# Kernel tuning notes

Hardware: AMD Instinct MI355X
Metric: run time of the kernel (lower is better)

Reference implementation:

```python
import jax, jax.numpy as jnp
import numpy as np

B, M, D, H = 2, 2048, 1024, 16


def _rope(x):
    # Equivalent to x.transpose(0,1) @ R[:m] with R the block-diagonal 2x2
    # rotation matrices from get_rotary_matrix (note the (i-1) in theta,
    # faithful to the source).
    b, m, d = x.shape
    i = jnp.arange(d // 2, dtype=jnp.float32)
    theta = 10000.0 ** (-2.0 * (i - 1.0) / d)           # [d/2]
    ang = jnp.arange(m, dtype=jnp.float32)[:, None] * theta[None, :]  # [m, d/2]
    c, s = jnp.cos(ang), jnp.sin(ang)
    xe, xo = x[..., 0::2], x[..., 1::2]                 # [b, m, d/2]
    ye = xe * c + xo * s                                # out[2i]   = q[2i]*cos + q[2i+1]*sin
    yo = -xe * s + xo * c                               # out[2i+1] = -q[2i]*sin + q[2i+1]*cos
    return jnp.stack([ye, yo], axis=-1).reshape(b, m, d)


def setup_inputs() -> dict:
    key = jax.random.key(0)
    ks = jax.random.split(key, 8)
    w = lambda k, shape: (jax.random.normal(k, shape, jnp.float32) * 0.02)
    return {
        "x": jax.random.normal(ks[0], (B, M, D), jnp.float32),
        "wq": w(ks[1], (D, D)),
        "wk": w(ks[2], (D, D)),
        "wv": w(ks[3], (D, D)),
        "in_proj_w": w(ks[4], (3 * D, D)),
        "in_proj_b": w(ks[5], (3 * D,)),
        "out_w": w(ks[6], (D, D)),
        "out_b": w(ks[7], (D,)),
    }


def reference(x, wq, wk, wv, in_proj_w, in_proj_b, out_w, out_b):
    b, m, d = x.shape
    h = H
    hd = d // h
    # bias-free QKV projections, each followed by the dense RoPE rotation
    q = _rope(x @ wq.T)
    k = _rope(x @ wk.T)
    v = _rope(x @ wv.T)
    # nn.MultiheadAttention: packed in_proj, scaled dot-product, causal mask, out_proj
    wqi, wki, wvi = jnp.split(in_proj_w, 3, axis=0)
    bqi, bki, bvi = jnp.split(in_proj_b, 3, axis=0)
    qh = (q @ wqi.T + bqi).reshape(b, m, h, hd)
    kh = (k @ wki.T + bki).reshape(b, m, h, hd)
    vh = (v @ wvi.T + bvi).reshape(b, m, h, hd)
    scores = jnp.einsum("bqhd,bkhd->bhqk", qh, kh) / jnp.sqrt(jnp.float32(hd))
    causal = jnp.tril(jnp.ones((m, m), dtype=bool))
    scores = jnp.where(causal, scores, jnp.float32(-jnp.inf))
    attn = jax.nn.softmax(scores, axis=-1)              # dropout p=0.0
    o = jnp.einsum("bhqk,bkhd->bqhd", attn, vh).reshape(b, m, d)
    return o @ out_w.T + out_b
```

## Files before the change

kernel.cpp:

```cpp
#include <hip/hip_runtime.h>
#include <hip/hip_bf16.h>
#include <math.h>

typedef __bf16 bf16;
typedef __bf16 bf16x4 __attribute__((ext_vector_type(4)));
typedef __bf16 bf16x8 __attribute__((ext_vector_type(8)));
typedef float  f32x4  __attribute__((ext_vector_type(4)));

#define MM 2048
#define DD 1024
#define HD 64

__device__ __forceinline__ void gload16(const void* g, void* l) {
  __builtin_amdgcn_global_load_lds((const __attribute__((address_space(1))) void*)g,
                                   (__attribute__((address_space(3))) void*)l, 16, 0, 0);
}

__global__ __launch_bounds__(256) void k_cvt_all(
    const float* __restrict__ x,   const float* __restrict__ wq,
    const float* __restrict__ wk,  const float* __restrict__ wv,
    const float* __restrict__ ipw, const float* __restrict__ ow,
    bf16* __restrict__ xb,  bf16* __restrict__ wqb, bf16* __restrict__ wkb,
    bf16* __restrict__ wvb, bf16* __restrict__ ipwb, bf16* __restrict__ owb)
{
  int bid = blockIdx.x;
  const float* s; bf16* d; int base;
  if (bid < 4096)       { s = x;   d = xb;   base = bid; }
  else if (bid < 5120)  { s = wq;  d = wqb;  base = bid - 4096; }
  else if (bid < 6144)  { s = wk;  d = wkb;  base = bid - 5120; }
  else if (bid < 7168)  { s = wv;  d = wvb;  base = bid - 6144; }
  else if (bid < 10240) { s = ipw; d = ipwb; base = bid - 7168; }
  else                  { s = ow;  d = owb;  base = bid - 10240; }
  int i = base*256 + threadIdx.x;
  float4 v = ((const float4*)s)[i];
  bf16x4 o;
  o[0]=(bf16)v.x; o[1]=(bf16)v.y; o[2]=(bf16)v.z; o[3]=(bf16)v.w;
  ((bf16x4*)d)[i] = o;
}

__device__ __forceinline__ void gemm_core8(const bf16* __restrict__ A,
                                           const bf16* __restrict__ Bw,
                                           const int row0, const int col0,
                                           bf16* __restrict__ sA, bf16* __restrict__ sB,
                                           f32x4 (&acc)[2][4])
{
  const int t = threadIdx.x;
  #pragma unroll
  for (int m=0;m<2;m++)
    #pragma unroll
    for (int n=0;n<4;n++)
      acc[m][n] = (f32x4){0.f,0.f,0.f,0.f};

  const int srow = t >> 3;
  const int lch  = ((t & 7) - (srow & 7)) & 7;
  const bf16* gA = A  + (size_t)(row0 + srow)*DD + lch*8;
  const bf16* gB = Bw + (size_t)(col0 + srow)*DD + lch*8;
  char* lA = (char*)sA + t*16;
  char* lB = (char*)sB + t*16;

  const int lane = t & 63, wid = t >> 6;
  const int wr = wid >> 1, wc = wid & 1;
  const int fr = lane & 15, fg = lane >> 4;
  const int fr7 = fr & 7;

  gload16(gA,                 lA);
  gload16(gA + (size_t)64*DD, lA + 8192);
  gload16(gB,                 lB);
  gload16(gB + (size_t)64*DD, lB + 8192);

  for (int kt = 0; kt < 16; ++kt) {
    const int buf = kt & 1;
    __builtin_amdgcn_s_barrier();
    if (kt < 15) {
      const int nb = buf ^ 1;
      const int ko = (kt + 1) * 64;
      gload16(gA + ko,                 lA + nb*16384);
      gload16(gA + (size_t)64*DD + ko, lA + nb*16384 + 8192);
      gload16(gB + ko,                 lB + nb*16384);
      gload16(gB + (size_t)64*DD + ko, lB + nb*16384 + 8192);
      asm volatile("s_waitcnt vmcnt(4)" ::: "memory");
    } else {
      asm volatile("s_waitcnt vmcnt(0)" ::: "memory");
    }
    __builtin_amdgcn_s_barrier();
    const char* bA = (const char*)sA + buf*16384;
    const char* bB = (const char*)sB + buf*16384;
    bf16x8 aF[2][2], bF[2][4];
    #pragma unroll
    for (int kb=0;kb<2;kb++) {
      #pragma unroll
      for (int m=0;m<2;m++)
        aF[kb][m] = *(const bf16x8*)(bA + (wr*32 + m*16 + fr)*128 + ((kb*4 + fg + fr7)&7)*16);
      #pragma unroll
      for (int n=0;n<4;n++)
        bF[kb][n] = *(const bf16x8*)(bB + (wc*64 + n*16 + fr)*128 + ((kb*4 + fg + fr7)&7)*16);
    }
    __builtin_amdgcn_s_setprio(1);
    #pragma unroll
    for (int kb=0;kb<2;kb++)
      #pragma unroll
      for (int m=0;m<2;m++)
        #pragma unroll
        for (int n=0;n<4;n++)
          acc[m][n] = __builtin_amdgcn_mfma_f32_16x16x32_bf16(aF[kb][m], bF[kb][n], acc[m][n], 0, 0, 0);
    __builtin_amdgcn_s_setprio(0);
  }
}

__global__ __launch_bounds__(512, 2) void k_gemm_rope(
    const bf16* __restrict__ X, const bf16* __restrict__ Wq,
    const bf16* __restrict__ Wk, const bf16* __restrict__ Wv,
    bf16* __restrict__ QKV)
{
  __shared__ bf16 sA[2*128*64];
  __shared__ bf16 sB[2*128*64];
  const int row0 = blockIdx.x * 128;
  const int col0 = blockIdx.y * 128;
  const int z = blockIdx.z;
  const bf16* Bw = (z==0) ? Wq : ((z==1) ? Wk : Wv);
  f32x4 acc[2][4];
  gemm_core8(X, Bw, row0, col0, sA, sB, acc);

  bf16* outp = QKV + (size_t)z * (4096u*1024u);
  const int lane = threadIdx.x & 63, wid = threadIdx.x >> 6;
  const int wr = wid >> 1, wc = wid & 1;
  const int fr = lane & 15, fg = lane >> 4;
  #pragma unroll
  for (int n=0;n<4;n++) {
    const int gc = col0 + wc*64 + n*16 + fr;
    const int i2 = gc >> 1;
    const float theta = __expf(((float)i2 - 1.0f) * (-2.0f * 9.210340371976184f / 1024.0f));
    #pragma unroll
    for (int m=0;m<2;m++) {
      #pragma unroll
      for (int r=0;r<4;r++) {
        const int gr = row0 + wr*32 + m*16 + fg*4 + r;
        const float v  = acc[m][n][r];
        const float pv = __shfl_xor(v, 1);
        const int pos = gr & (MM-1);
        float sv, cv;
        __sincosf((float)pos * theta, &sv, &cv);
        const float res = (gc & 1) ? (v*cv - pv*sv) : (v*cv + pv*sv);
        outp[(size_t)gr * DD + gc] = (bf16)res;
      }
    }
  }
}

__global__ __launch_bounds__(512, 2) void k_gemm_proj(
    const bf16* __restrict__ QKV, const bf16* __restrict__ IPW,
    const float* __restrict__ IPB,
    bf16* __restrict__ QH, bf16* __restrict__ KH, bf16* __restrict__ VT)
{
  __shared__ bf16 sA[2*128*64];
  __shared__ bf16 sB[2*128*64];
  const int row0 = blockIdx.x * 128;
  const int col0 = blockIdx.y * 128;
  const int z = blockIdx.z;
  const bf16* A  = QKV + (size_t)z * (4096u*1024u);
  const bf16* Bw = IPW + (size_t)z * (1024u*1024u);
  const float* bias = IPB + z * DD;
  f32x4 acc[2][4];
  gemm_core8(A, Bw, row0, col0, sA, sB, acc);

  const int lane = threadIdx.x & 63, wid = threadIdx.x >> 6;
  const int wr = wid >> 1, wc = wid & 1;
  const int fr = lane & 15, fg = lane >> 4;
  if (z < 2) {
    bf16* outp = (z==0) ? QH : KH;
    const float vscale = (z==0) ? 0.18033688011112042f : 1.0f;
    #pragma unroll
    for (int n=0;n<4;n++) {
      const int gc = col0 + wc*64 + n*16 + fr;
      const float bs = bias[gc];
      #pragma unroll
      for (int m=0;m<2;m++) {
        #pragma unroll
        for (int r=0;r<4;r++) {
          const int gr = row0 + wr*32 + m*16 + fg*4 + r;
          outp[(size_t)gr * DD + gc] = (bf16)((acc[m][n][r] + bs) * vscale);
        }
      }
    }
  } else {
    #pragma unroll
    for (int n=0;n<4;n++) {
      const int gc = col0 + wc*64 + n*16 + fr;
      const float bs = bias[gc];
      #pragma unroll
      for (int m=0;m<2;m++) {
        const int gr0 = row0 + wr*32 + m*16 + fg*4;
        const int b  = gr0 >> 11;
        const int m0 = gr0 & (MM-1);
        bf16x4 pk;
        #pragma unroll
        for (int r=0;r<4;r++) pk[r] = (bf16)(acc[m][n][r] + bs);
        *(bf16x4*)(VT + ((size_t)b*DD + gc)*MM + m0) = pk;
      }
    }
  }
}

__global__ __launch_bounds__(256) void k_attn(
    const bf16* __restrict__ QH, const bf16* __restrict__ KH,
    const bf16* __restrict__ VT, bf16* __restrict__ O)
{
  __shared__ bf16 sK[2*64*64];
  __shared__ bf16 sV[2*64*64];
  __shared__ bf16 sP[4*16*64];
  const int idx = blockIdx.x;
  const int xcd = idx & 7;
  const int rr  = idx >> 3;
  const int combo = xcd*4 + (rr & 3);
  const int b = combo >> 4, h = combo & 15;
  const int qt = 31 - (rr >> 2);
  const int t = threadIdx.x, lane = t & 63, wid = t >> 6;
  const int fr = lane & 15, fg = lane >> 4;
  const int swzP = (fr & 7) << 4;
  const int q0 = qt * 64;
  const int qg = q0 + wid*16 + fr;

  const int srow = t >> 3;
  const int cc   = (t & 7) ^ (srow & 7);
  const bf16* gK0 = KH + ((size_t)b*MM + srow)*DD + h*HD + cc*8;
  const bf16* gK1 = gK0 + (size_t)32*DD;
  const bf16* gV0 = VT + ((size_t)b*DD + h*HD + srow)*MM + cc*8;
  const bf16* gV1 = gV0 + (size_t)32*MM;
  char* lK = (char*)sK + t*16;
  char* lV = (char*)sV + t*16;
  char* sPw = (char*)(sP + wid*16*64);

  const bf16* qp = QH + ((size_t)b*MM + qg)*DD + h*HD + fg*8;
  bf16x8 aQ0 = *(const bf16x8*)qp;
  bf16x8 aQ1 = *(const bf16x8*)(qp + 32);

  bf16x8 ones;
  #pragma unroll
  for (int j=0;j<8;j++) ones[j] = (bf16)1.0f;

  gload16(gK0, lK);  gload16(gK1, lK + 4096);
  gload16(gV0, lV);  gload16(gV1, lV + 4096);

  f32x4 o_acc[4];
  #pragma unroll
  for (int n=0;n<4;n++) o_acc[n] = (f32x4){0.f,0.f,0.f,0.f};
  f32x4 lacc = (f32x4){0.f,0.f,0.f,0.f};
  const f32x4 minit = (f32x4){-32.f,-32.f,-32.f,-32.f};

  for (int kt = 0; kt <= qt; ++kt) {
    const int buf = kt & 1;
    asm volatile("s_waitcnt vmcnt(0)" ::: "memory");
    __builtin_amdgcn_s_barrier();
    if (kt < qt) {
      const int nb = buf ^ 1;
      gload16(gK0 + (size_t)(kt+1)*64*DD, lK + nb*8192);
      gload16(gK1 + (size_t)(kt+1)*64*DD, lK + nb*8192 + 4096);
      gload16(gV0 + (kt+1)*64,            lV + nb*8192);
      gload16(gV1 + (kt+1)*64,            lV + nb*8192 + 4096);
    }
    const char* bKb = (const char*)sK + buf*8192;
    const char* bVb = (const char*)sV + buf*8192;

    f32x4 sacc[4];
    #pragma unroll
    for (int n=0;n<4;n++) sacc[n] = minit;
    __builtin_amdgcn_s_setprio(1);
    #pragma unroll
    for (int kb=0;kb<2;kb++) {
      const bf16x8 q = kb ? aQ1 : aQ0;
      #pragma unroll
      for (int n=0;n<4;n++) {
        const int rowA = n*16 + fr;
        bf16x8 aK = *(const bf16x8*)(bKb + rowA*128 + ((kb*64 + fg*16) ^ ((rowA&7)<<4)));
        sacc[n] = __builtin_amdgcn_mfma_f32_16x16x32_bf16(aK, q, sacc[n], 0, 0, 0);
      }
    }
    __builtin_amdgcn_s_setprio(0);

    const bool diag = (kt == qt);
    float ps[16];
    #pragma unroll
    for (int n=0;n<4;n++)
      #pragma unroll
      for (int r=0;r<4;r++) {
        float xx = sacc[n][r];
        if (diag) {
          const int kvg = kt*64 + n*16 + fg*4 + r;
          if (kvg > qg) xx = -INFINITY;
        }
        ps[n*4+r] = exp2f(xx);
      }
    #pragma unroll
    for (int n=0;n<4;n++) {
      bf16x4 pk;
      #pragma unroll
      for (int r=0;r<4;r++) pk[r] = (bf16)ps[n*4+r];
      *(bf16x4*)(sPw + fr*128 + ((n*32 + fg*8) ^ swzP)) = pk;
    }
    asm volatile("s_waitcnt lgkmcnt(0)" ::: "memory");

    bf16x8 aP0 = *(const bf16x8*)(sPw + fr*128 + ((fg*16) ^ swzP));
    bf16x8 aP1 = *(const bf16x8*)(sPw + fr*128 + ((64 + fg*16) ^ swzP));
    __builtin_amdgcn_s_setprio(1);
    #pragma unroll
    for (int n=0;n<4;n++) {
      const int rowV = n*16 + fr;
      bf16x8 bV0 = *(const bf16x8*)(bVb + rowV*128 + ((fg*16) ^ ((rowV&7)<<4)));
      bf16x8 bV1 = *(const bf16x8*)(bVb + rowV*128 + ((64 + fg*16) ^ ((rowV&7)<<4)));
      o_acc[n] = __builtin_amdgcn_mfma_f32_16x16x32_bf16(aP0, bV0, o_acc[n], 0, 0, 0);
      o_acc[n] = __builtin_amdgcn_mfma_f32_16x16x32_bf16(aP1, bV1, o_acc[n], 0, 0, 0);
    }
    lacc = __builtin_amdgcn_mfma_f32_16x16x32_bf16(aP0, ones, lacc, 0, 0, 0);
    lacc = __builtin_amdgcn_mfma_f32_16x16x32_bf16(aP1, ones, lacc, 0, 0, 0);
    __builtin_amdgcn_s_setprio(0);
  }

  #pragma unroll
  for (int r=0;r<4;r++) {
    const int qq = q0 + wid*16 + fg*4 + r;
    const float inv = 1.0f / lacc[r];
    #pragma unroll
    for (int n=0;n<4;n++) {
      O[((size_t)b*MM + qq)*DD + h*HD + n*16 + fr] = (bf16)(o_acc[n][r] * inv);
    }
  }
}

__global__ __launch_bounds__(512, 2) void k_gemm_out(
    const bf16* __restrict__ A, const bf16* __restrict__ OW,
    const float* __restrict__ OBIAS, float* __restrict__ outp)
{
  __shared__ bf16 sA[2*128*64];
  __shared__ bf16 sB[2*128*64];
  const int row0 = blockIdx.x * 128;
  const int col0 = blockIdx.y * 128;
  f32x4 acc[2][4];
  gemm_core8(A, OW, row0, col0, sA, sB, acc);
  const int lane = threadIdx.x & 63, wid = threadIdx.x >> 6;
  const int wr = wid >> 1, wc = wid & 1;
  const int fr = lane & 15, fg = lane >> 4;
  #pragma unroll
  for (int n=0;n<4;n++) {
    const int gc = col0 + wc*64 + n*16 + fr;
    const float bs = OBIAS[gc];
    #pragma unroll
    for (int m=0;m<2;m++) {
      #pragma unroll
      for (int r=0;r<4;r++) {
        const int gr = row0 + wr*32 + m*16 + fg*4 + r;
        outp[(size_t)gr * DD + gc] = acc[m][n][r] + bs;
      }
    }
  }
}

extern "C" void kernel_launch(void* const* d_in, const int* in_sizes, int n_in,
                              void* d_out, int out_size, void* d_ws, size_t ws_size,
                              hipStream_t stream)
{
  (void)in_sizes; (void)n_in; (void)out_size; (void)ws_size;
  const float* x   = (const float*)d_in[0];
  const float* wq  = (const float*)d_in[1];
  const float* wk  = (const float*)d_in[2];
  const float* wv  = (const float*)d_in[3];
  const float* ipw = (const float*)d_in[4];
  const float* ipb = (const float*)d_in[5];
  const float* ow  = (const float*)d_in[6];
  const float* ob  = (const float*)d_in[7];
  float* outp = (float*)d_out;

  char* ws = (char*)d_ws;
  const size_t MB = 1u << 20;
  bf16* xb   = (bf16*)(ws + 0*MB);
  bf16* wqb  = (bf16*)(ws + 8*MB);
  bf16* wkb  = (bf16*)(ws + 10*MB);
  bf16* wvb  = (bf16*)(ws + 12*MB);
  bf16* ipwb = (bf16*)(ws + 14*MB);
  bf16* owb  = (bf16*)(ws + 20*MB);
  bf16* QKV  = (bf16*)(ws + 22*MB);
  bf16* QH   = (bf16*)(ws + 46*MB);
  bf16* KH   = (bf16*)(ws + 54*MB);
  bf16* VT   = (bf16*)(ws + 62*MB);
  bf16* Ob   = (bf16*)(ws + 70*MB);

  k_cvt_all<<<11264, 256, 0, stream>>>(x, wq, wk, wv, ipw, ow,
                                       xb, wqb, wkb, wvb, ipwb, owb);
  k_gemm_rope<<<dim3(32,8,3), 512, 0, stream>>>(xb, wqb, wkb, wvb, QKV);
  k_gemm_proj<<<dim3(32,8,3), 512, 0, stream>>>(QKV, ipwb, ipb, QH, KH, VT);
  k_attn<<<1024, 256, 0, stream>>>(QH, KH, VT, Ob);
  k_gemm_out<<<dim3(32,8,1), 512, 0, stream>>>(Ob, owb, ob, outp);
}
```

Measured before the change: 128.7 us.

## Split long causal attention query tiles into two KV halves with merge kernel

Query tiles 16-31 now have their KV loop split at tile 16 into two blocks, each writing unnormalised fp32 partial outputs and row sums to a workspace that reuses the QKV buffer. A new merge kernel sums the two partials and normalises them. The aim is to balance the causal workload across more blocks (1536 instead of 1024) and shorten the critical path of the longest tiles. The cost is an extra kernel launch and fp32 partial traffic. The merge is valid because the softmax uses a fixed max offset rather than a running max.

```diff
diff --git a/kernel.cpp b/kernel.cpp
--- a/kernel.cpp
+++ b/kernel.cpp
@@ -203,7 +203,8 @@
 
 __global__ __launch_bounds__(256) void k_attn(
     const bf16* __restrict__ QH, const bf16* __restrict__ KH,
-    const bf16* __restrict__ VT, bf16* __restrict__ O)
+    const bf16* __restrict__ VT, bf16* __restrict__ O,
+    float* __restrict__ pOut)
 {
   __shared__ bf16 sK[2*64*64];
   __shared__ bf16 sV[2*64*64];
@@ -213,7 +214,13 @@
   const int rr  = idx >> 3;
   const int combo = xcd*4 + (rr & 3);
   const int b = combo >> 4, h = combo & 15;
-  const int qt = 31 - (rr >> 2);
+  const int u = rr >> 2;
+  int qt, kt0, ktEnd, mode, slot = 0;
+  if (u < 16)      { qt = 16 + u; kt0 = 0;  ktEnd = 15; mode = 1;
+                     slot = (combo*16 + u)*2; }
+  else if (u < 32) { qt = 31 - u; kt0 = 0;  ktEnd = qt; mode = 0; }
+  else             { qt = 63 - u; kt0 = 16; ktEnd = qt; mode = 1;
+                     slot = (combo*16 + (qt-16))*2 + 1; }
   const int t = threadIdx.x, lane = t & 63, wid = t >> 6;
   const int fr = lane & 15, fg = lane >> 4;
   const int swzP = (fr & 7) << 4;
@@ -238,8 +245,8 @@
   #pragma unroll
   for (int j=0;j<8;j++) ones[j] = (bf16)1.0f;
 
-  gload16(gK0, lK);  gload16(gK1, lK + 4096);
-  gload16(gV0, lV);  gload16(gV1, lV + 4096);
+  gload16(gK0 + (size_t)kt0*64*DD, lK);  gload16(gK1 + (size_t)kt0*64*DD, lK + 4096);
+  gload16(gV0 + kt0*64, lV);             gload16(gV1 + kt0*64, lV + 4096);
 
   f32x4 o_acc[4];
   #pragma unroll
@@ -247,11 +254,11 @@
   f32x4 lacc = (f32x4){0.f,0.f,0.f,0.f};
   const f32x4 minit = (f32x4){-32.f,-32.f,-32.f,-32.f};
 
-  for (int kt = 0; kt <= qt; ++kt) {
+  for (int kt = kt0; kt <= ktEnd; ++kt) {
     const int buf = kt & 1;
     asm volatile("s_waitcnt vmcnt(0)" ::: "memory");
     __builtin_amdgcn_s_barrier();
-    if (kt < qt) {
+    if (kt < ktEnd) {
       const int nb = buf ^ 1;
       gload16(gK0 + (size_t)(kt+1)*64*DD, lK + nb*8192);
       gload16(gK1 + (size_t)(kt+1)*64*DD, lK + nb*8192 + 4096);
@@ -315,14 +322,43 @@
     __builtin_amdgcn_s_setprio(0);
   }
 
-  #pragma unroll
-  for (int r=0;r<4;r++) {
-    const int qq = q0 + wid*16 + fg*4 + r;
-    const float inv = 1.0f / lacc[r];
-    #pragma unroll
-    for (int n=0;n<4;n++) {
-      O[((size_t)b*MM + qq)*DD + h*HD + n*16 + fr] = (bf16)(o_acc[n][r] * inv);
-    }
+  if (mode == 0) {
+    #pragma unroll
+    for (int r=0;r<4;r++) {
+      const int qq = q0 + wid*16 + fg*4 + r;
+      const float inv = 1.0f / lacc[r];
+      #pragma unroll
+      for (int n=0;n<4;n++) {
+        O[((size_t)b*MM + qq)*DD + h*HD + n*16 + fr] = (bf16)(o_acc[n][r] * inv);
+      }
+    }
+  } else {
+    float* po = pOut + (size_t)slot * 4160;
+    #pragma unroll
+    for (int r=0;r<4;r++) {
+      const int row = wid*16 + fg*4 + r;
+      #pragma unroll
+      for (int n=0;n<4;n++) po[row*64 + n*16 + fr] = o_acc[n][r];
+      if (fr == 0) po[4096 + row] = lacc[r];
+    }
+  }
+}
+
+__global__ __launch_bounds__(256) void k_attn_merge(
+    const float* __restrict__ pOut, bf16* __restrict__ O)
+{
+  const int m = blockIdx.x;
+  const int combo = m >> 4;
+  const int b = combo >> 4, h = combo & 15;
+  const int qt = 16 + (m & 15);
+  const float* pa = pOut + (size_t)(m*2)   * 4160;
+  const float* pb = pOut + (size_t)(m*2+1) * 4160;
+  const int t = threadIdx.x;
+  const int col = t & 63;
+  for (int row = t >> 6; row < 64; row += 4) {
+    const float inv = 1.0f / (pa[4096 + row] + pb[4096 + row]);
+    const float o = (pa[row*64 + col] + pb[row*64 + col]) * inv;
+    O[((size_t)b*MM + qt*64 + row)*DD + h*HD + col] = (bf16)o;
   }
 }
 
@@ -378,6 +414,7 @@
   bf16* ipwb = (bf16*)(ws + 14*MB);
   bf16* owb  = (bf16*)(ws + 20*MB);
   bf16* QKV  = (bf16*)(ws + 22*MB);
+  float* pO  = (float*)(ws + 22*MB);
   bf16* QH   = (bf16*)(ws + 46*MB);
   bf16* KH   = (bf16*)(ws + 54*MB);
   bf16* VT   = (bf16*)(ws + 62*MB);
@@ -387,6 +424,7 @@
                                        xb, wqb, wkb, wvb, ipwb, owb);
   k_gemm_rope<<<dim3(32,8,3), 512, 0, stream>>>(xb, wqb, wkb, wvb, QKV);
   k_gemm_proj<<<dim3(32,8,3), 512, 0, stream>>>(QKV, ipwb, ipb, QH, KH, VT);
-  k_attn<<<1024, 256, 0, stream>>>(QH, KH, VT, Ob);
+  k_attn<<<1536, 256, 0, stream>>>(QH, KH, VT, Ob, pO);
+  k_attn_merge<<<512, 256, 0, stream>>>(pO, Ob);
   k_gemm_out<<<dim3(32,8,1), 512, 0, stream>>>(Ob, owb, ob, outp);
 }
```

Result: slower. 135.3 us (+5.2%).
